# Kernel tuning notes

Measured on AMD Instinct MI355X. Metric: run time of the kernel, lower is better.

Reference implementation:

```python
import jax, jax.numpy as jnp
import numpy as np

DT = 0.1  # module buffer `dt`
I_DIM, H_DIM, BATCH, SEQ = 128, 64, 8, 4096


def setup_inputs() -> dict:
    key = jax.random.key(0)
    ks = jax.random.split(key, 6)
    return {
        "x": jax.random.normal(ks[0], (BATCH, SEQ, I_DIM), dtype=jnp.float32),
        "B": jax.random.uniform(ks[1], (I_DIM, H_DIM), dtype=jnp.float32),
        "C_tilde": jax.random.uniform(ks[2], (I_DIM, H_DIM), dtype=jnp.float32),
        "Lambda": jax.random.uniform(ks[3], (I_DIM, 1, H_DIM), dtype=jnp.float32),
        "P": jax.random.uniform(ks[4], (I_DIM, H_DIM), dtype=jnp.float32),
        "Q": jax.random.uniform(ks[5], (I_DIM, H_DIM), dtype=jnp.float32),
    }


def _compute_K(B, C_tilde, Lambda, P, Q, L):
    # omega_k = exp(2*pi*i*k/L), k = 0..L-1
    n = jnp.arange(L, dtype=jnp.float32)
    omega = jnp.exp((2j * jnp.pi / L) * n).astype(jnp.complex64)          # [L]
    g = (2.0 / DT) * ((1.0 - omega) / (1.0 + omega))                      # [L]
    # denominator: [I, L, H] complex (the big intermediate)
    inv = 1.0 / (g[None, :, None] - Lambda.astype(jnp.complex64))
    a0, a1 = jnp.conj(C_tilde), Q                                          # [I, H]
    b0, b1 = B, P                                                          # [I, H]
    # Cauchy dot products: sum over hidden dim -> [I, L]
    k00 = jnp.einsum('ih,ilh->il', (a0 * b0).astype(jnp.complex64), inv)
    k01 = jnp.einsum('ih,ilh->il', (a0 * b1).astype(jnp.complex64), inv)
    k10 = jnp.einsum('ih,ilh->il', (a1 * b0).astype(jnp.complex64), inv)
    k11 = jnp.einsum('ih,ilh->il', (a1 * b1).astype(jnp.complex64), inv)
    c = 2.0 / (1.0 + omega)                                                # [L]
    K_hat = c[None, :] * (k00 - k01 * (1.0 + k11) * k10)                   # [I, L]
    # irfft crops input along last axis to L//2 + 1 bins (matches torch)
    return jnp.fft.irfft(K_hat, n=L, axis=-1)                              # [I, L] real


def reference(x, B, C_tilde, Lambda, P, Q):
    Bz, L, I = x.shape
    K = _compute_K(B, C_tilde, Lambda, P, Q, L)        # [I, L]
    xt = jnp.transpose(x, (0, 2, 1))                   # [B, I, L]
    n2 = 2 * L
    x_fft = jnp.fft.rfft(xt, n=n2, axis=2)             # zero-pad to 2L -> [B, I, L+1]
    K_fft = jnp.fft.rfft(K, n=n2, axis=1)[None]        # [1, I, L+1]
    y = jnp.fft.irfft(x_fft * K_fft, n=n2, axis=2)[:, :, :L]
    return jnp.transpose(y, (0, 2, 1))                 # [B, L, I]
```

## Files before the change

kernel.cpp:

```cpp
#include <hip/hip_runtime.h>

#define I_DIM 128
#define H_DIM 64
#define BATCH 8
#define SEQ   4096
#define NBIN  (SEQ/2 + 1)
#define NBIN2 (SEQ + 1)

#define SZ(a) ((a) ^ (((a) >> 4) & 15))

__device__ float  g_xT[(size_t)BATCH * I_DIM * SEQ];
__device__ float2 g_Hh[I_DIM * NBIN];
__device__ float2 g_Kf[I_DIM * NBIN2];
__device__ float2 g_Xf[(size_t)BATCH * I_DIM * SEQ];
__device__ float  g_Yt[(size_t)BATCH * I_DIM * SEQ];

__device__ inline float2 cmul(float2 a, float2 b) {
    return make_float2(a.x * b.x - a.y * b.y, a.x * b.y + a.y * b.x);
}
__device__ inline float2 cadd(float2 a, float2 b) { return make_float2(a.x + b.x, a.y + b.y); }
__device__ inline float2 csub(float2 a, float2 b) { return make_float2(a.x - b.x, a.y - b.y); }

__device__ inline void dft8(float2 a[8]) {
    const float C = 0.70710678118654752f;
    float2 s0 = cadd(a[0], a[4]), s1 = cadd(a[1], a[5]);
    float2 s2 = cadd(a[2], a[6]), s3 = cadd(a[3], a[7]);
    float2 d0 = csub(a[0], a[4]), d1 = csub(a[1], a[5]);
    float2 d2 = csub(a[2], a[6]), d3 = csub(a[3], a[7]);
    d1 = make_float2(C * (d1.x + d1.y), C * (d1.y - d1.x));
    d2 = make_float2(d2.y, -d2.x);
    d3 = make_float2(C * (d3.y - d3.x), -C * (d3.x + d3.y));
    {
        float2 p0 = cadd(s0, s2), p1 = cadd(s1, s3);
        float2 m0 = csub(s0, s2), m1 = csub(s1, s3);
        m1 = make_float2(m1.y, -m1.x);
        a[0] = cadd(p0, p1); a[4] = csub(p0, p1);
        a[2] = cadd(m0, m1); a[6] = csub(m0, m1);
    }
    {
        float2 p0 = cadd(d0, d2), p1 = cadd(d1, d3);
        float2 m0 = csub(d0, d2), m1 = csub(d1, d3);
        m1 = make_float2(m1.y, -m1.x);
        a[1] = cadd(p0, p1); a[5] = csub(p0, p1);
        a[3] = cadd(m0, m1); a[7] = csub(m0, m1);
    }
}

__device__ inline void dft4(float2 a[4]) {
    float2 p0 = cadd(a[0], a[2]), p1 = cadd(a[1], a[3]);
    float2 m0 = csub(a[0], a[2]), m1 = csub(a[1], a[3]);
    m1 = make_float2(m1.y, -m1.x);
    a[0] = cadd(p0, p1); a[2] = csub(p0, p1);
    a[1] = cadd(m0, m1); a[3] = csub(m0, m1);
}

template <int N, int S, int NT>
__device__ inline void stage8(float2* __restrict__ lds, int tid) {
    constexpr int NB = N / 8;
    constexpr int ITER = (NB + NT - 1) / NT;
    const bool act = (NB >= NT) || (tid < NB);
    float2 d[ITER][8];
#pragma unroll
    for (int b = 0; b < ITER; ++b) {
        const int u = tid + b * NT;
        if (act) {
#pragma unroll
            for (int j = 0; j < 8; ++j)
                d[b][j] = lds[SZ(u + NB * j)];
        }
    }
    __syncthreads();
#pragma unroll
    for (int b = 0; b < ITER; ++b) {
        const int u = tid + b * NT;
        if (act) {
            const int q = u & (S - 1);
            dft8(d[b]);
            if constexpr (S < NB) {
                const float cang = (float)(-6.283185307179586) / (float)N;
                float sn, cs;
                __sincosf(cang * (float)(u - q), &sn, &cs);
                const float2 w = make_float2(cs, sn);
                float2 t = w;
#pragma unroll
                for (int k = 1; k < 8; ++k) {
                    d[b][k] = cmul(d[b][k], t);
                    if (k < 7) t = cmul(t, w);
                }
            }
            const int base = 8 * u - 7 * q;
#pragma unroll
            for (int k = 0; k < 8; ++k)
                lds[SZ(base + k * S)] = d[b][k];
        }
    }
    __syncthreads();
}

template <int N, int S, int NT>
__device__ inline void stage4(float2* __restrict__ lds, int tid) {
    constexpr int NB = N / 4;
    constexpr int ITER = (NB + NT - 1) / NT;
    const bool act = (NB >= NT) || (tid < NB);
    float2 d[ITER][4];
#pragma unroll
    for (int b = 0; b < ITER; ++b) {
        const int u = tid + b * NT;
        if (act) {
#pragma unroll
            for (int j = 0; j < 4; ++j)
                d[b][j] = lds[SZ(u + NB * j)];
        }
    }
    __syncthreads();
#pragma unroll
    for (int b = 0; b < ITER; ++b) {
        const int u = tid + b * NT;
        if (act) {
            const int q = u & (S - 1);
            dft4(d[b]);
            if constexpr (S < NB) {
                const float cang = (float)(-6.283185307179586) / (float)N;
                float sn, cs;
                __sincosf(cang * (float)(u - q), &sn, &cs);
                const float2 w = make_float2(cs, sn);
                float2 t = w;
#pragma unroll
                for (int k = 1; k < 4; ++k) {
                    d[b][k] = cmul(d[b][k], t);
                    if (k < 3) t = cmul(t, w);
                }
            }
            const int base = 4 * u - 3 * q;
#pragma unroll
            for (int k = 0; k < 4; ++k)
                lds[SZ(base + k * S)] = d[b][k];
        }
    }
    __syncthreads();
}

__device__ inline void halfzero4096_writeback(float2* __restrict__ lds, int tid,
                                              float2 a0, float2 a1,
                                              float2 a2, float2 a3) {
    const float C = 0.70710678118654752f;
    __syncthreads();
    float2 p0 = cadd(a0, a2), p1 = cadd(a1, a3);
    float2 m0 = csub(a0, a2), m1t = csub(a1, a3);
    float2 m1 = make_float2(m1t.y, -m1t.x);
    float2 b0 = cadd(p0, p1), b4 = csub(p0, p1);
    float2 b2 = cadd(m0, m1), b6 = csub(m0, m1);
    float2 c1 = make_float2(C * (a1.x + a1.y), C * (a1.y - a1.x));
    float2 c2 = make_float2(a2.y, -a2.x);
    float2 c3 = make_float2(C * (a3.y - a3.x), -C * (a3.x + a3.y));
    float2 q0 = cadd(a0, c2), q1 = cadd(c1, c3);
    float2 n0 = csub(a0, c2), n1t = csub(c1, c3);
    float2 n1 = make_float2(n1t.y, -n1t.x);
    float2 b1 = cadd(q0, q1), b5 = csub(q0, q1);
    float2 b3 = cadd(n0, n1), b7 = csub(n0, n1);
    float sn, cs;
    __sincosf((float)(-6.283185307179586 / 4096.0) * (float)tid, &sn, &cs);
    float2 w1 = make_float2(cs, sn);
    float2 w2 = cmul(w1, w1), w3 = cmul(w2, w1), w4 = cmul(w2, w2);
    float2 w5 = cmul(w3, w2), w6 = cmul(w3, w3), w7 = cmul(w4, w3);
    const int base = 8 * tid;
    lds[SZ(base + 0)] = b0;
    lds[SZ(base + 1)] = cmul(b1, w1);
    lds[SZ(base + 2)] = cmul(b2, w2);
    lds[SZ(base + 3)] = cmul(b3, w3);
    lds[SZ(base + 4)] = cmul(b4, w4);
    lds[SZ(base + 5)] = cmul(b5, w5);
    lds[SZ(base + 6)] = cmul(b6, w6);
    lds[SZ(base + 7)] = cmul(b7, w7);
    __syncthreads();
}

__device__ inline float2 khat_bin(int i, int k,
                                  const float* __restrict__ Bm,
                                  const float* __restrict__ Cm,
                                  const float* __restrict__ Lm,
                                  const float* __restrict__ Pm,
                                  const float* __restrict__ Qm) {
    float theta = (float)(6.283185307179586 / (double)SEQ) * (float)k;
    float sn, cs;
    sincosf(theta, &sn, &cs);
    float tr = 1.0f - cs, ti = -sn;
    float br = 1.0f + cs, bi = sn;
    float idn = 1.0f / (br * br + bi * bi);
    float gr = 20.0f * (tr * br + ti * bi) * idn;
    float gi = 20.0f * (ti * br - tr * bi) * idn;
    float cr = 2.0f * br * idn;
    float ci = -2.0f * bi * idn;

    const float* Brow = Bm + i * H_DIM;
    const float* Crow = Cm + i * H_DIM;
    const float* Lrow = Lm + i * H_DIM;
    const float* Prow = Pm + i * H_DIM;
    const float* Qrow = Qm + i * H_DIM;

    float k00r = 0.f, k00i = 0.f, k01r = 0.f, k01i = 0.f;
    float k10r = 0.f, k10i = 0.f, k11r = 0.f, k11i = 0.f;
#pragma unroll 8
    for (int h = 0; h < H_DIM; ++h) {
        float lam = Lrow[h];
        float drr = gr - lam;
        float dii = gi;
        float im = 1.0f / (drr * drr + dii * dii);
        float ivr = drr * im;
        float ivi = -dii * im;
        float bv = Brow[h], cv = Crow[h], pv = Prow[h], qv = Qrow[h];
        float cb = cv * bv;
        float cp = cv * pv;
        float qb = qv * bv;
        float qp = qv * pv;
        k00r += cb * ivr; k00i += cb * ivi;
        k01r += cp * ivr; k01i += cp * ivi;
        k10r += qb * ivr; k10i += qb * ivi;
        k11r += qp * ivr; k11i += qp * ivi;
    }
    float t1r = 1.0f + k11r, t1i = k11i;
    float t2r = k01r * t1r - k01i * t1i;
    float t2i = k01r * t1i + k01i * t1r;
    float t3r = t2r * k10r - t2i * k10i;
    float t3i = t2r * k10i + t2i * k10r;
    float nr = k00r - t3r, ni = k00i - t3i;
    return make_float2(cr * nr - ci * ni, cr * ni + ci * nr);
}

__global__ __launch_bounds__(256) void k1_transpose_khat(const float* __restrict__ x,
                                                         const float* __restrict__ Bm,
                                                         const float* __restrict__ Cm,
                                                         const float* __restrict__ Lm,
                                                         const float* __restrict__ Pm,
                                                         const float* __restrict__ Qm) {
    __shared__ float t[64][65];
    const int blk = blockIdx.x;
    const int b = blk >> 7;
    const int rest = blk & 127;
    const int nt = rest >> 1;
    const int it = rest & 1;
    const int tx = threadIdx.x & 63;
    const int ty = threadIdx.x >> 6;
    const int n0 = nt * 64, i0 = it * 64;

    const float* xb = x + (size_t)b * SEQ * I_DIM;
#pragma unroll
    for (int r = 0; r < 16; ++r) {
        int nl = r * 4 + ty;
        t[nl][tx] = xb[(size_t)(n0 + nl) * I_DIM + i0 + tx];
    }
    __syncthreads();
#pragma unroll
    for (int r = 0; r < 16; ++r) {
        int il = r * 4 + ty;
        g_xT[((size_t)b * I_DIM + i0 + il) * SEQ + n0 + tx] = t[tx][il];
    }

    const int ch = blk >> 3, sl = blk & 7;
    const int k = sl * 256 + threadIdx.x;
    g_Hh[(size_t)ch * NBIN + k] = khat_bin(ch, k, Bm, Cm, Lm, Pm, Qm);
    if (sl == 0 && threadIdx.x == 0)
        g_Hh[(size_t)ch * NBIN + 2048] = khat_bin(ch, 2048, Bm, Cm, Lm, Pm, Qm);
}

__global__ __launch_bounds__(512) void k2_kprep_fwd() {
    __shared__ float2 lds[4096];
    const int tid = threadIdx.x;

    if (blockIdx.x < I_DIM) {
        const int i = blockIdx.x;
        const float2* Hrow = g_Hh + (size_t)i * NBIN;
#pragma unroll
        for (int r = 0; r < 4; ++r) {
            int m = tid + (r << 9);
            float2 Hm = Hrow[m];
            float2 Hc = Hrow[2048 - m];
            float pr = Hm.x + Hc.x, pi2 = Hm.y - Hc.y;
            float dr = Hm.x - Hc.x, di = Hm.y + Hc.y;
            float sn, cs;
            __sincosf((float)(3.141592653589793 / 2048.0) * (float)m, &sn, &cs);
            float Or = 0.5f * (cs * dr - sn * di);
            float Oi = 0.5f * (sn * dr + cs * di);
            lds[SZ(m)] = make_float2(0.5f * pr - Oi, -(0.5f * pi2 + Or));
        }
        __syncthreads();

        stage4<2048, 1,   512>(lds, tid);
        stage8<2048, 4,   512>(lds, tid);
        stage8<2048, 32,  512>(lds, tid);
        stage8<2048, 256, 512>(lds, tid);

        const float s1 = 1.0f / 2048.0f;
        float2 a[4];
#pragma unroll
        for (int j = 0; j < 4; ++j) {
            float2 o = lds[SZ(tid + (j << 9))];
            a[j] = make_float2(o.x * s1, -o.y * s1);
        }
        halfzero4096_writeback(lds, tid, a[0], a[1], a[2], a[3]);

        stage8<4096, 8,   512>(lds, tid);
        stage8<4096, 64,  512>(lds, tid);
        stage8<4096, 512, 512>(lds, tid);

        float2* Kfrow = g_Kf + (size_t)i * NBIN2;
#pragma unroll
        for (int r = 0; r < 9; ++r) {
            int m = tid + (r << 9);
            if (m <= 4096) {
                float2 Zq = lds[SZ(m & 4095)];
                float2 Zr = lds[SZ((4096 - m) & 4095)];
                float sn, cs;
                __sincosf((float)(-3.141592653589793 / 4096.0) * (float)m, &sn, &cs);
                float pr = Zq.x + Zr.x, pi2 = Zq.y - Zr.y;
                float dr = Zq.x - Zr.x, di = Zq.y + Zr.y;
                float jt_r = -sn * dr - cs * di;
                float jt_i =  cs * dr - sn * di;
                Kfrow[m] = make_float2(0.5f * (pr - jt_r), 0.5f * (pi2 - jt_i));
            }
        }
    } else {
        const int blk = blockIdx.x - I_DIM;
        const int b = blk & 7;
        const int i = blk >> 3;

        const float2* xrow = (const float2*)(g_xT + ((size_t)b * I_DIM + i) * SEQ);
        float2 a0 = xrow[tid];
        float2 a1 = xrow[tid + 512];
        float2 a2 = xrow[tid + 1024];
        float2 a3 = xrow[tid + 1536];
        halfzero4096_writeback(lds, tid, a0, a1, a2, a3);

        stage8<4096, 8,  512>(lds, tid);
        stage8<4096, 64, 512>(lds, tid);

        float2 e[8];
#pragma unroll
        for (int j = 0; j < 8; ++j) e[j] = lds[SZ(tid + (j << 9))];
        dft8(e);
        float2* dst = g_Xf + (size_t)blk * SEQ;
#pragma unroll
        for (int k = 0; k < 8; ++k)
            dst[tid + (k << 9)] = e[k];
    }
}

__global__ __launch_bounds__(512) void k3_combine_inv() {
    __shared__ float2 lds[4096];
    const int tid = threadIdx.x;
    const int blk = blockIdx.x;
    const int b = blk & 7;
    const int i = blk >> 3;
    const float2* Xf = g_Xf + (size_t)blk * SEQ;
    const float2* Kfrow = g_Kf + (size_t)i * NBIN2;

    float2 d[8];
#pragma unroll
    for (int j = 0; j < 8; ++j) {
        int m = tid + (j << 9);
        int mm = (4096 - m) & 4095;
        float2 Zq = Xf[m];
        float2 Zr = Xf[mm];
        float2 Km  = Kfrow[m];
        float2 Km2 = Kfrow[4096 - m];
        float sn, cs;
        __sincosf((float)(-3.141592653589793 / 4096.0) * (float)m, &sn, &cs);
        float pr = Zq.x + Zr.x, pi2 = Zq.y - Zr.y;
        float dr = Zq.x - Zr.x, di = Zq.y + Zr.y;
        float jt_r = -sn * dr - cs * di;
        float jt_i =  cs * dr - sn * di;
        float2 Xm  = make_float2(0.5f * (pr - jt_r),  0.5f * ( pi2 - jt_i));
        float2 Xm2 = make_float2(0.5f * (pr + jt_r),  0.5f * (-pi2 - jt_i));
        float2 Ym  = cmul(Xm,  Km);
        float2 Ym2 = cmul(Xm2, Km2);
        float qr = Ym.x + Ym2.x, qi = Ym.y - Ym2.y;
        float er = Ym.x - Ym2.x, ei = Ym.y + Ym2.y;
        float gr2 = sn * er - cs * ei;
        float gi2 = sn * ei + cs * er;
        d[j] = make_float2(0.5f * (qr + gr2), -0.5f * (qi + gi2));
    }

    dft8(d);
    {
        float sn, cs;
        __sincosf((float)(-6.283185307179586 / 4096.0) * (float)tid, &sn, &cs);
        float2 w1 = make_float2(cs, sn);
        float2 w2 = cmul(w1, w1), w3 = cmul(w2, w1), w4 = cmul(w2, w2);
        float2 w5 = cmul(w3, w2), w6 = cmul(w3, w3), w7 = cmul(w4, w3);
        d[1] = cmul(d[1], w1); d[2] = cmul(d[2], w2); d[3] = cmul(d[3], w3);
        d[4] = cmul(d[4], w4); d[5] = cmul(d[5], w5); d[6] = cmul(d[6], w6);
        d[7] = cmul(d[7], w7);
    }
    const int base = 8 * tid;
#pragma unroll
    for (int k = 0; k < 8; ++k) lds[SZ(base + k)] = d[k];
    __syncthreads();

    stage8<4096, 8,  512>(lds, tid);
    stage8<4096, 64, 512>(lds, tid);

    float2 e[8];
#pragma unroll
    for (int j = 0; j < 8; ++j) e[j] = lds[SZ(tid + (j << 9))];
    dft8(e);
    const float inv = 1.0f / 4096.0f;
    float2* yrow = (float2*)(g_Yt + ((size_t)b * I_DIM + i) * SEQ);
#pragma unroll
    for (int k = 0; k < 4; ++k)
        yrow[tid + (k << 9)] = make_float2(e[k].x * inv, -e[k].y * inv);
}

__global__ __launch_bounds__(256) void k4_transpose_out(float* __restrict__ y) {
    __shared__ float t[64][65];
    const int blk = blockIdx.x;
    const int b = blk >> 7;
    const int rest = blk & 127;
    const int nt = rest >> 1;
    const int it = rest & 1;
    const int tx = threadIdx.x & 63;
    const int ty = threadIdx.x >> 6;
    const int n0 = nt * 64, i0 = it * 64;

#pragma unroll
    for (int r = 0; r < 16; ++r) {
        int il = r * 4 + ty;
        t[il][tx] = g_Yt[((size_t)b * I_DIM + i0 + il) * SEQ + n0 + tx];
    }
    __syncthreads();
    float* yb = y + (size_t)b * SEQ * I_DIM;
#pragma unroll
    for (int r = 0; r < 16; ++r) {
        int nl = r * 4 + ty;
        yb[(size_t)(n0 + nl) * I_DIM + i0 + tx] = t[tx][nl];
    }
}

extern "C" void kernel_launch(void* const* d_in, const int* in_sizes, int n_in,
                              void* d_out, int out_size, void* d_ws, size_t ws_size,
                              hipStream_t stream) {
    const float* x  = (const float*)d_in[0];
    const float* Bm = (const float*)d_in[1];
    const float* Cm = (const float*)d_in[2];
    const float* Lm = (const float*)d_in[3];
    const float* Pm = (const float*)d_in[4];
    const float* Qm = (const float*)d_in[5];
    float* out = (float*)d_out;

    k1_transpose_khat<<<1024, 256, 0, stream>>>(x, Bm, Cm, Lm, Pm, Qm);
    k2_kprep_fwd<<<I_DIM + BATCH * I_DIM, 512, 0, stream>>>();
    k3_combine_inv<<<BATCH * I_DIM, 512, 0, stream>>>();
    k4_transpose_out<<<1024, 256, 0, stream>>>(out);
}
```

Measured before the change: 72.17 us.

## Pack two real channels per complex FFT instead of real-FFT half-length trick

Replaces the half-length real-FFT packing (one real row as a 4096-point complex FFT plus post-twiddle) with a two-for-one scheme: channel g and g+64 are packed as real and imaginary parts of one 8192-point complex FFT, and their spectra are split by conjugate symmetry. The kernel-spectrum, forward-x and inverse passes all switch to 8192-point transforms with 64KB of LDS, and the block count halves. This drops the separate twiddle pre- and post-processing passes and gives each block more work, at the cost of doubled LDS per block (lower occupancy), an extra radix stage, and more scattered conjugate-index global reads.

```diff
diff --git a/kernel.cpp b/kernel.cpp
--- a/kernel.cpp
+++ b/kernel.cpp
@@ -46,14 +46,6 @@
     }
 }
 
-__device__ inline void dft4(float2 a[4]) {
-    float2 p0 = cadd(a[0], a[2]), p1 = cadd(a[1], a[3]);
-    float2 m0 = csub(a[0], a[2]), m1 = csub(a[1], a[3]);
-    m1 = make_float2(m1.y, -m1.x);
-    a[0] = cadd(p0, p1); a[2] = csub(p0, p1);
-    a[1] = cadd(m0, m1); a[3] = csub(m0, m1);
-}
-
 template <int N, int S, int NT>
 __device__ inline void stage8(float2* __restrict__ lds, int tid) {
     constexpr int NB = N / 8;
@@ -97,54 +89,11 @@
     __syncthreads();
 }
 
-template <int N, int S, int NT>
-__device__ inline void stage4(float2* __restrict__ lds, int tid) {
-    constexpr int NB = N / 4;
-    constexpr int ITER = (NB + NT - 1) / NT;
-    const bool act = (NB >= NT) || (tid < NB);
-    float2 d[ITER][4];
-#pragma unroll
-    for (int b = 0; b < ITER; ++b) {
-        const int u = tid + b * NT;
-        if (act) {
-#pragma unroll
-            for (int j = 0; j < 4; ++j)
-                d[b][j] = lds[SZ(u + NB * j)];
-        }
-    }
-    __syncthreads();
-#pragma unroll
-    for (int b = 0; b < ITER; ++b) {
-        const int u = tid + b * NT;
-        if (act) {
-            const int q = u & (S - 1);
-            dft4(d[b]);
-            if constexpr (S < NB) {
-                const float cang = (float)(-6.283185307179586) / (float)N;
-                float sn, cs;
-                __sincosf(cang * (float)(u - q), &sn, &cs);
-                const float2 w = make_float2(cs, sn);
-                float2 t = w;
-#pragma unroll
-                for (int k = 1; k < 4; ++k) {
-                    d[b][k] = cmul(d[b][k], t);
-                    if (k < 3) t = cmul(t, w);
-                }
-            }
-            const int base = 4 * u - 3 * q;
-#pragma unroll
-            for (int k = 0; k < 4; ++k)
-                lds[SZ(base + k * S)] = d[b][k];
-        }
-    }
-    __syncthreads();
-}
-
-__device__ inline void halfzero4096_writeback(float2* __restrict__ lds, int tid,
-                                              float2 a0, float2 a1,
-                                              float2 a2, float2 a3) {
+template <int N>
+__device__ inline void halfzero_s1_write(float2* __restrict__ lds, int u,
+                                         float2 a0, float2 a1,
+                                         float2 a2, float2 a3) {
     const float C = 0.70710678118654752f;
-    __syncthreads();
     float2 p0 = cadd(a0, a2), p1 = cadd(a1, a3);
     float2 m0 = csub(a0, a2), m1t = csub(a1, a3);
     float2 m1 = make_float2(m1t.y, -m1t.x);
@@ -159,11 +108,11 @@
     float2 b1 = cadd(q0, q1), b5 = csub(q0, q1);
     float2 b3 = cadd(n0, n1), b7 = csub(n0, n1);
     float sn, cs;
-    __sincosf((float)(-6.283185307179586 / 4096.0) * (float)tid, &sn, &cs);
+    __sincosf((float)(-6.283185307179586) / (float)N * (float)u, &sn, &cs);
     float2 w1 = make_float2(cs, sn);
     float2 w2 = cmul(w1, w1), w3 = cmul(w2, w1), w4 = cmul(w2, w2);
     float2 w5 = cmul(w3, w2), w6 = cmul(w3, w3), w7 = cmul(w4, w3);
-    const int base = 8 * tid;
+    const int base = 8 * u;
     lds[SZ(base + 0)] = b0;
     lds[SZ(base + 1)] = cmul(b1, w1);
     lds[SZ(base + 2)] = cmul(b2, w2);
@@ -172,7 +121,25 @@
     lds[SZ(base + 5)] = cmul(b5, w5);
     lds[SZ(base + 6)] = cmul(b6, w6);
     lds[SZ(base + 7)] = cmul(b7, w7);
-    __syncthreads();
+}
+
+template <int N>
+__device__ inline void full_s1_write(float2* __restrict__ lds, int u, float2 d[8]) {
+    dft8(d);
+    float sn, cs;
+    __sincosf((float)(-6.283185307179586) / (float)N * (float)u, &sn, &cs);
+    float2 w1 = make_float2(cs, sn);
+    float2 w2 = cmul(w1, w1), w3 = cmul(w2, w1), w4 = cmul(w2, w2);
+    float2 w5 = cmul(w3, w2), w6 = cmul(w3, w3), w7 = cmul(w4, w3);
+    const int base = 8 * u;
+    lds[SZ(base + 0)] = d[0];
+    lds[SZ(base + 1)] = cmul(d[1], w1);
+    lds[SZ(base + 2)] = cmul(d[2], w2);
+    lds[SZ(base + 3)] = cmul(d[3], w3);
+    lds[SZ(base + 4)] = cmul(d[4], w4);
+    lds[SZ(base + 5)] = cmul(d[5], w5);
+    lds[SZ(base + 6)] = cmul(d[6], w6);
+    lds[SZ(base + 7)] = cmul(d[7], w7);
 }
 
 __device__ inline float2 khat_bin(int i, int k,
@@ -264,150 +231,166 @@
 }
 
 __global__ __launch_bounds__(512) void k2_kprep_fwd() {
-    __shared__ float2 lds[4096];
+    __shared__ float2 L[8192];
     const int tid = threadIdx.x;
 
-    if (blockIdx.x < I_DIM) {
-        const int i = blockIdx.x;
-        const float2* Hrow = g_Hh + (size_t)i * NBIN;
-#pragma unroll
-        for (int r = 0; r < 4; ++r) {
+    if (blockIdx.x < 64) {
+        const int g = blockIdx.x;
+        const float2* HA = g_Hh + (size_t)g * NBIN;
+        const float2* HB = g_Hh + (size_t)(g + 64) * NBIN;
+
+        float2 d[8];
+#pragma unroll
+        for (int j = 0; j < 8; ++j) {
+            int m = tid + (j << 9);
+            float2 hA, hB;
+            if (m <= 2048) { hA = HA[m]; hB = HB[m]; }
+            else {
+                float2 tA = HA[4096 - m], tB = HB[4096 - m];
+                hA = make_float2(tA.x, -tA.y);
+                hB = make_float2(tB.x, -tB.y);
+            }
+            d[j] = make_float2(hA.x - hB.y, -(hA.y + hB.x));
+        }
+        full_s1_write<4096>(L, tid, d);
+        __syncthreads();
+
+        stage8<4096, 8,   512>(L, tid);
+        stage8<4096, 64,  512>(L, tid);
+        stage8<4096, 512, 512>(L, tid);
+
+        const float s1 = 1.0f / 4096.0f;
+        float2 va[2][4];
+#pragma unroll
+        for (int b2 = 0; b2 < 2; ++b2)
+#pragma unroll
+            for (int j = 0; j < 4; ++j) {
+                int n = tid + (b2 << 9) + (j << 10);
+                float2 o = L[SZ(n)];
+                va[b2][j] = make_float2(o.x * s1, -o.y * s1);
+            }
+        __syncthreads();
+#pragma unroll
+        for (int b2 = 0; b2 < 2; ++b2)
+            halfzero_s1_write<8192>(L, tid + (b2 << 9),
+                                    va[b2][0], va[b2][1], va[b2][2], va[b2][3]);
+        __syncthreads();
+
+        stage8<8192, 8,   512>(L, tid);
+        stage8<8192, 64,  512>(L, tid);
+        stage8<8192, 512, 512>(L, tid);
+
+        float2* KfA = g_Kf + (size_t)g * NBIN2;
+        float2* KfB = g_Kf + (size_t)(g + 64) * NBIN2;
+#pragma unroll
+        for (int r = 0; r < 8; ++r) {
             int m = tid + (r << 9);
-            float2 Hm = Hrow[m];
-            float2 Hc = Hrow[2048 - m];
-            float pr = Hm.x + Hc.x, pi2 = Hm.y - Hc.y;
-            float dr = Hm.x - Hc.x, di = Hm.y + Hc.y;
-            float sn, cs;
-            __sincosf((float)(3.141592653589793 / 2048.0) * (float)m, &sn, &cs);
-            float Or = 0.5f * (cs * dr - sn * di);
-            float Oi = 0.5f * (sn * dr + cs * di);
-            lds[SZ(m)] = make_float2(0.5f * pr - Oi, -(0.5f * pi2 + Or));
-        }
+            float2 A0 = L[SZ(m)], A1 = L[SZ(m + 4096)];
+            float2 P = cadd(A0, A1);
+            float2 Q;
+            if (m == 0) Q = P;
+            else {
+                float2 B0 = L[SZ(4096 - m)], B1 = L[SZ(8192 - m)];
+                Q = csub(B0, B1);
+            }
+            KfA[m] = make_float2(0.5f * (P.x + Q.x), 0.5f * (P.y - Q.y));
+            float dxr = P.x - Q.x, dyr = P.y + Q.y;
+            KfB[m] = make_float2(0.5f * dyr, -0.5f * dxr);
+        }
+        if (tid == 0) {
+            float2 P = csub(L[SZ(0)], L[SZ(4096)]);
+            KfA[4096] = make_float2(P.x, 0.f);
+            KfB[4096] = make_float2(P.y, 0.f);
+        }
+    } else {
+        const int blk = blockIdx.x - 64;
+        const int b = blk & 7;
+        const int g = blk >> 3;
+        const float* xrA = g_xT + ((size_t)b * I_DIM + g) * SEQ;
+        const float* xrB = g_xT + ((size_t)b * I_DIM + g + 64) * SEQ;
+
+        float2 va[2][4];
+#pragma unroll
+        for (int b2 = 0; b2 < 2; ++b2)
+#pragma unroll
+            for (int j = 0; j < 4; ++j) {
+                int n = tid + (b2 << 9) + (j << 10);
+                va[b2][j] = make_float2(xrA[n], xrB[n]);
+            }
+#pragma unroll
+        for (int b2 = 0; b2 < 2; ++b2)
+            halfzero_s1_write<8192>(L, tid + (b2 << 9),
+                                    va[b2][0], va[b2][1], va[b2][2], va[b2][3]);
         __syncthreads();
 
-        stage4<2048, 1,   512>(lds, tid);
-        stage8<2048, 4,   512>(lds, tid);
-        stage8<2048, 32,  512>(lds, tid);
-        stage8<2048, 256, 512>(lds, tid);
-
-        const float s1 = 1.0f / 2048.0f;
-        float2 a[4];
-#pragma unroll
-        for (int j = 0; j < 4; ++j) {
-            float2 o = lds[SZ(tid + (j << 9))];
-            a[j] = make_float2(o.x * s1, -o.y * s1);
-        }
-        halfzero4096_writeback(lds, tid, a[0], a[1], a[2], a[3]);
-
-        stage8<4096, 8,   512>(lds, tid);
-        stage8<4096, 64,  512>(lds, tid);
-        stage8<4096, 512, 512>(lds, tid);
-
-        float2* Kfrow = g_Kf + (size_t)i * NBIN2;
-#pragma unroll
-        for (int r = 0; r < 9; ++r) {
-            int m = tid + (r << 9);
-            if (m <= 4096) {
-                float2 Zq = lds[SZ(m & 4095)];
-                float2 Zr = lds[SZ((4096 - m) & 4095)];
-                float sn, cs;
-                __sincosf((float)(-3.141592653589793 / 4096.0) * (float)m, &sn, &cs);
-                float pr = Zq.x + Zr.x, pi2 = Zq.y - Zr.y;
-                float dr = Zq.x - Zr.x, di = Zq.y + Zr.y;
-                float jt_r = -sn * dr - cs * di;
-                float jt_i =  cs * dr - sn * di;
-                Kfrow[m] = make_float2(0.5f * (pr - jt_r), 0.5f * (pi2 - jt_i));
-            }
-        }
-    } else {
-        const int blk = blockIdx.x - I_DIM;
-        const int b = blk & 7;
-        const int i = blk >> 3;
-
-        const float2* xrow = (const float2*)(g_xT + ((size_t)b * I_DIM + i) * SEQ);
-        float2 a0 = xrow[tid];
-        float2 a1 = xrow[tid + 512];
-        float2 a2 = xrow[tid + 1024];
-        float2 a3 = xrow[tid + 1536];
-        halfzero4096_writeback(lds, tid, a0, a1, a2, a3);
-
-        stage8<4096, 8,  512>(lds, tid);
-        stage8<4096, 64, 512>(lds, tid);
-
-        float2 e[8];
-#pragma unroll
-        for (int j = 0; j < 8; ++j) e[j] = lds[SZ(tid + (j << 9))];
-        dft8(e);
-        float2* dst = g_Xf + (size_t)blk * SEQ;
-#pragma unroll
-        for (int k = 0; k < 8; ++k)
-            dst[tid + (k << 9)] = e[k];
+        stage8<8192, 8,   512>(L, tid);
+        stage8<8192, 64,  512>(L, tid);
+        stage8<8192, 512, 512>(L, tid);
+
+        float2* dst = g_Xf + (size_t)blk * 2 * SEQ;
+#pragma unroll
+        for (int r = 0; r < 8; ++r) {
+            int u = tid + (r << 9);
+            float2 A0 = L[SZ(u)], A1 = L[SZ(u + 4096)];
+            dst[u]        = cadd(A0, A1);
+            dst[u + 4096] = csub(A0, A1);
+        }
     }
 }
 
 __global__ __launch_bounds__(512) void k3_combine_inv() {
-    __shared__ float2 lds[4096];
+    __shared__ float2 L[8192];
     const int tid = threadIdx.x;
     const int blk = blockIdx.x;
     const int b = blk & 7;
-    const int i = blk >> 3;
-    const float2* Xf = g_Xf + (size_t)blk * SEQ;
-    const float2* Kfrow = g_Kf + (size_t)i * NBIN2;
-
-    float2 d[8];
-#pragma unroll
-    for (int j = 0; j < 8; ++j) {
-        int m = tid + (j << 9);
-        int mm = (4096 - m) & 4095;
-        float2 Zq = Xf[m];
-        float2 Zr = Xf[mm];
-        float2 Km  = Kfrow[m];
-        float2 Km2 = Kfrow[4096 - m];
-        float sn, cs;
-        __sincosf((float)(-3.141592653589793 / 4096.0) * (float)m, &sn, &cs);
-        float pr = Zq.x + Zr.x, pi2 = Zq.y - Zr.y;
-        float dr = Zq.x - Zr.x, di = Zq.y + Zr.y;
-        float jt_r = -sn * dr - cs * di;
-        float jt_i =  cs * dr - sn * di;
-        float2 Xm  = make_float2(0.5f * (pr - jt_r),  0.5f * ( pi2 - jt_i));
-        float2 Xm2 = make_float2(0.5f * (pr + jt_r),  0.5f * (-pi2 - jt_i));
-        float2 Ym  = cmul(Xm,  Km);
-        float2 Ym2 = cmul(Xm2, Km2);
-        float qr = Ym.x + Ym2.x, qi = Ym.y - Ym2.y;
-        float er = Ym.x - Ym2.x, ei = Ym.y + Ym2.y;
-        float gr2 = sn * er - cs * ei;
-        float gi2 = sn * ei + cs * er;
-        d[j] = make_float2(0.5f * (qr + gr2), -0.5f * (qi + gi2));
-    }
-
-    dft8(d);
-    {
-        float sn, cs;
-        __sincosf((float)(-6.283185307179586 / 4096.0) * (float)tid, &sn, &cs);
-        float2 w1 = make_float2(cs, sn);
-        float2 w2 = cmul(w1, w1), w3 = cmul(w2, w1), w4 = cmul(w2, w2);
-        float2 w5 = cmul(w3, w2), w6 = cmul(w3, w3), w7 = cmul(w4, w3);
-        d[1] = cmul(d[1], w1); d[2] = cmul(d[2], w2); d[3] = cmul(d[3], w3);
-        d[4] = cmul(d[4], w4); d[5] = cmul(d[5], w5); d[6] = cmul(d[6], w6);
-        d[7] = cmul(d[7], w7);
-    }
-    const int base = 8 * tid;
-#pragma unroll
-    for (int k = 0; k < 8; ++k) lds[SZ(base + k)] = d[k];
+    const int g = blk >> 3;
+    const float2* Z = g_Xf + (size_t)blk * 2 * SEQ;
+    const float2* KfA = g_Kf + (size_t)g * NBIN2;
+    const float2* KfB = g_Kf + (size_t)(g + 64) * NBIN2;
+
+    float2 d[2][8];
+#pragma unroll
+    for (int b2 = 0; b2 < 2; ++b2) {
+        const int u = tid + (b2 << 9);
+#pragma unroll
+        for (int j = 0; j < 8; ++j) {
+            int m = u + (j << 10);
+            float2 P = Z[m];
+            float2 Q = (m == 0) ? P : Z[8192 - m];
+            float2 XA = make_float2(0.5f * (P.x + Q.x), 0.5f * (P.y - Q.y));
+            float dxr = P.x - Q.x, dyr = P.y + Q.y;
+            float2 XB = make_float2(0.5f * dyr, -0.5f * dxr);
+            float2 KA, KB;
+            if (m <= 4096) { KA = KfA[m]; KB = KfB[m]; }
+            else {
+                float2 tA = KfA[8192 - m], tB = KfB[8192 - m];
+                KA = make_float2(tA.x, -tA.y);
+                KB = make_float2(tB.x, -tB.y);
+            }
+            float2 YA = cmul(XA, KA);
+            float2 YB = cmul(XB, KB);
+            d[b2][j] = make_float2(YA.x - YB.y, -(YA.y + YB.x));
+        }
+    }
+#pragma unroll
+    for (int b2 = 0; b2 < 2; ++b2)
+        full_s1_write<8192>(L, tid + (b2 << 9), d[b2]);
     __syncthreads();
 
-    stage8<4096, 8,  512>(lds, tid);
-    stage8<4096, 64, 512>(lds, tid);
-
-    float2 e[8];
-#pragma unroll
-    for (int j = 0; j < 8; ++j) e[j] = lds[SZ(tid + (j << 9))];
-    dft8(e);
-    const float inv = 1.0f / 4096.0f;
-    float2* yrow = (float2*)(g_Yt + ((size_t)b * I_DIM + i) * SEQ);
-#pragma unroll
-    for (int k = 0; k < 4; ++k)
-        yrow[tid + (k << 9)] = make_float2(e[k].x * inv, -e[k].y * inv);
+    stage8<8192, 8,   512>(L, tid);
+    stage8<8192, 64,  512>(L, tid);
+    stage8<8192, 512, 512>(L, tid);
+
+    const float inv = 1.0f / 8192.0f;
+    float* yA = g_Yt + ((size_t)b * I_DIM + g) * SEQ;
+    float* yB = g_Yt + ((size_t)b * I_DIM + g + 64) * SEQ;
+#pragma unroll
+    for (int r = 0; r < 8; ++r) {
+        int n = tid + (r << 9);
+        float2 F = cadd(L[SZ(n)], L[SZ(n + 4096)]);
+        yA[n] = F.x * inv;
+        yB[n] = -F.y * inv;
+    }
 }
 
 __global__ __launch_bounds__(256) void k4_transpose_out(float* __restrict__ y) {
@@ -447,7 +430,7 @@
     float* out = (float*)d_out;
 
     k1_transpose_khat<<<1024, 256, 0, stream>>>(x, Bm, Cm, Lm, Pm, Qm);
-    k2_kprep_fwd<<<I_DIM + BATCH * I_DIM, 512, 0, stream>>>();
-    k3_combine_inv<<<BATCH * I_DIM, 512, 0, stream>>>();
+    k2_kprep_fwd<<<64 + 512, 512, 0, stream>>>();
+    k3_combine_inv<<<512, 512, 0, stream>>>();
     k4_transpose_out<<<1024, 256, 0, stream>>>(out);
 }
```

Result: slower. 82.91 us (+14.9%).

## Switch 4096-point FFTs to radix-16 stages with 256-thread blocks

Applied to the files above, without the earlier changes.

Replaces the radix-8/radix-4 LDS FFT stages with radix-16 stages run by 256 threads, cutting the number of LDS round trips and barriers per 4096-point transform from about three to two. The K spectrum path is restructured: a 4096-point inverse of the Hermitian half-spectrum, followed by a twiddled forward transform that only fills the odd bins, while even bins are copied straight from Hh. The LDS swizzle gains an extra XOR term to avoid bank conflicts at the larger strides. Each thread now holds 16 complex values, which raises register pressure and may reduce occupancy.

```diff
diff --git a/kernel.cpp b/kernel.cpp
--- a/kernel.cpp
+++ b/kernel.cpp
@@ -7,7 +7,7 @@
 #define NBIN  (SEQ/2 + 1)
 #define NBIN2 (SEQ + 1)
 
-#define SZ(a) ((a) ^ (((a) >> 4) & 15))
+#define SZ(a) ((a) ^ (((a) >> 4) & 15) ^ (((a) >> 8) & 15))
 
 __device__ float  g_xT[(size_t)BATCH * I_DIM * SEQ];
 __device__ float2 g_Hh[I_DIM * NBIN];
@@ -46,132 +46,105 @@
     }
 }
 
-__device__ inline void dft4(float2 a[4]) {
-    float2 p0 = cadd(a[0], a[2]), p1 = cadd(a[1], a[3]);
-    float2 m0 = csub(a[0], a[2]), m1 = csub(a[1], a[3]);
-    m1 = make_float2(m1.y, -m1.x);
-    a[0] = cadd(p0, p1); a[2] = csub(p0, p1);
-    a[1] = cadd(m0, m1); a[3] = csub(m0, m1);
-}
-
-template <int N, int S, int NT>
-__device__ inline void stage8(float2* __restrict__ lds, int tid) {
-    constexpr int NB = N / 8;
-    constexpr int ITER = (NB + NT - 1) / NT;
-    const bool act = (NB >= NT) || (tid < NB);
-    float2 d[ITER][8];
-#pragma unroll
-    for (int b = 0; b < ITER; ++b) {
-        const int u = tid + b * NT;
-        if (act) {
-#pragma unroll
-            for (int j = 0; j < 8; ++j)
-                d[b][j] = lds[SZ(u + NB * j)];
-        }
-    }
-    __syncthreads();
-#pragma unroll
-    for (int b = 0; b < ITER; ++b) {
-        const int u = tid + b * NT;
-        if (act) {
-            const int q = u & (S - 1);
-            dft8(d[b]);
-            if constexpr (S < NB) {
-                const float cang = (float)(-6.283185307179586) / (float)N;
-                float sn, cs;
-                __sincosf(cang * (float)(u - q), &sn, &cs);
-                const float2 w = make_float2(cs, sn);
-                float2 t = w;
-#pragma unroll
-                for (int k = 1; k < 8; ++k) {
-                    d[b][k] = cmul(d[b][k], t);
-                    if (k < 7) t = cmul(t, w);
-                }
-            }
-            const int base = 8 * u - 7 * q;
-#pragma unroll
-            for (int k = 0; k < 8; ++k)
-                lds[SZ(base + k * S)] = d[b][k];
-        }
-    }
-    __syncthreads();
-}
-
-template <int N, int S, int NT>
-__device__ inline void stage4(float2* __restrict__ lds, int tid) {
-    constexpr int NB = N / 4;
-    constexpr int ITER = (NB + NT - 1) / NT;
-    const bool act = (NB >= NT) || (tid < NB);
-    float2 d[ITER][4];
-#pragma unroll
-    for (int b = 0; b < ITER; ++b) {
-        const int u = tid + b * NT;
-        if (act) {
-#pragma unroll
-            for (int j = 0; j < 4; ++j)
-                d[b][j] = lds[SZ(u + NB * j)];
-        }
-    }
-    __syncthreads();
-#pragma unroll
-    for (int b = 0; b < ITER; ++b) {
-        const int u = tid + b * NT;
-        if (act) {
-            const int q = u & (S - 1);
-            dft4(d[b]);
-            if constexpr (S < NB) {
-                const float cang = (float)(-6.283185307179586) / (float)N;
-                float sn, cs;
-                __sincosf(cang * (float)(u - q), &sn, &cs);
-                const float2 w = make_float2(cs, sn);
-                float2 t = w;
-#pragma unroll
-                for (int k = 1; k < 4; ++k) {
-                    d[b][k] = cmul(d[b][k], t);
-                    if (k < 3) t = cmul(t, w);
-                }
-            }
-            const int base = 4 * u - 3 * q;
-#pragma unroll
-            for (int k = 0; k < 4; ++k)
-                lds[SZ(base + k * S)] = d[b][k];
-        }
-    }
-    __syncthreads();
-}
-
-__device__ inline void halfzero4096_writeback(float2* __restrict__ lds, int tid,
-                                              float2 a0, float2 a1,
-                                              float2 a2, float2 a3) {
+__device__ inline void dft8hz(float2 x0, float2 x1, float2 x2, float2 x3,
+                              float2 b[8]) {
     const float C = 0.70710678118654752f;
-    __syncthreads();
-    float2 p0 = cadd(a0, a2), p1 = cadd(a1, a3);
-    float2 m0 = csub(a0, a2), m1t = csub(a1, a3);
+    float2 p0 = cadd(x0, x2), p1 = cadd(x1, x3);
+    float2 m0 = csub(x0, x2), m1t = csub(x1, x3);
     float2 m1 = make_float2(m1t.y, -m1t.x);
-    float2 b0 = cadd(p0, p1), b4 = csub(p0, p1);
-    float2 b2 = cadd(m0, m1), b6 = csub(m0, m1);
-    float2 c1 = make_float2(C * (a1.x + a1.y), C * (a1.y - a1.x));
-    float2 c2 = make_float2(a2.y, -a2.x);
-    float2 c3 = make_float2(C * (a3.y - a3.x), -C * (a3.x + a3.y));
-    float2 q0 = cadd(a0, c2), q1 = cadd(c1, c3);
-    float2 n0 = csub(a0, c2), n1t = csub(c1, c3);
+    b[0] = cadd(p0, p1); b[4] = csub(p0, p1);
+    b[2] = cadd(m0, m1); b[6] = csub(m0, m1);
+    float2 c1 = make_float2(C * (x1.x + x1.y), C * (x1.y - x1.x));
+    float2 c2 = make_float2(x2.y, -x2.x);
+    float2 c3 = make_float2(C * (x3.y - x3.x), -C * (x3.x + x3.y));
+    float2 q0 = cadd(x0, c2), q1 = cadd(c1, c3);
+    float2 n0 = csub(x0, c2), n1t = csub(c1, c3);
     float2 n1 = make_float2(n1t.y, -n1t.x);
-    float2 b1 = cadd(q0, q1), b5 = csub(q0, q1);
-    float2 b3 = cadd(n0, n1), b7 = csub(n0, n1);
+    b[1] = cadd(q0, q1); b[5] = csub(q0, q1);
+    b[3] = cadd(n0, n1); b[7] = csub(n0, n1);
+}
+
+__device__ inline void combine16(const float2 e[8], const float2 o[8],
+                                 float2 b[16]) {
+    const float C  = 0.70710678118654752f;
+    const float C1 = 0.92387953251128674f;
+    const float S1 = 0.38268343236508977f;
+    float2 t;
+    b[0] = cadd(e[0], o[0]);  b[8]  = csub(e[0], o[0]);
+    t = cmul(o[1], make_float2( C1, -S1)); b[1] = cadd(e[1], t); b[9]  = csub(e[1], t);
+    t = cmul(o[2], make_float2(  C,  -C)); b[2] = cadd(e[2], t); b[10] = csub(e[2], t);
+    t = cmul(o[3], make_float2( S1, -C1)); b[3] = cadd(e[3], t); b[11] = csub(e[3], t);
+    t = make_float2(o[4].y, -o[4].x);      b[4] = cadd(e[4], t); b[12] = csub(e[4], t);
+    t = cmul(o[5], make_float2(-S1, -C1)); b[5] = cadd(e[5], t); b[13] = csub(e[5], t);
+    t = cmul(o[6], make_float2( -C,  -C)); b[6] = cadd(e[6], t); b[14] = csub(e[6], t);
+    t = cmul(o[7], make_float2(-C1, -S1)); b[7] = cadd(e[7], t); b[15] = csub(e[7], t);
+}
+
+__device__ inline void dft16(float2 a[16]) {
+    float2 e[8] = {a[0], a[2], a[4], a[6], a[8], a[10], a[12], a[14]};
+    float2 o[8] = {a[1], a[3], a[5], a[7], a[9], a[11], a[13], a[15]};
+    dft8(e); dft8(o);
+    combine16(e, o, a);
+}
+
+__device__ inline void s1_twiddle_write(float2* __restrict__ lds, int u,
+                                        float2 b[16]) {
     float sn, cs;
-    __sincosf((float)(-6.283185307179586 / 4096.0) * (float)tid, &sn, &cs);
+    __sincosf((float)(-6.283185307179586 / 4096.0) * (float)u, &sn, &cs);
     float2 w1 = make_float2(cs, sn);
     float2 w2 = cmul(w1, w1), w3 = cmul(w2, w1), w4 = cmul(w2, w2);
     float2 w5 = cmul(w3, w2), w6 = cmul(w3, w3), w7 = cmul(w4, w3);
-    const int base = 8 * tid;
-    lds[SZ(base + 0)] = b0;
-    lds[SZ(base + 1)] = cmul(b1, w1);
-    lds[SZ(base + 2)] = cmul(b2, w2);
-    lds[SZ(base + 3)] = cmul(b3, w3);
-    lds[SZ(base + 4)] = cmul(b4, w4);
-    lds[SZ(base + 5)] = cmul(b5, w5);
-    lds[SZ(base + 6)] = cmul(b6, w6);
-    lds[SZ(base + 7)] = cmul(b7, w7);
+    float2 w8 = cmul(w4, w4);
+    const int base = 16 * u;
+    lds[SZ(base + 0)]  = b[0];
+    lds[SZ(base + 1)]  = cmul(b[1], w1);
+    lds[SZ(base + 2)]  = cmul(b[2], w2);
+    lds[SZ(base + 3)]  = cmul(b[3], w3);
+    lds[SZ(base + 4)]  = cmul(b[4], w4);
+    lds[SZ(base + 5)]  = cmul(b[5], w5);
+    lds[SZ(base + 6)]  = cmul(b[6], w6);
+    lds[SZ(base + 7)]  = cmul(b[7], w7);
+    lds[SZ(base + 8)]  = cmul(b[8], w8);
+    lds[SZ(base + 9)]  = cmul(cmul(b[9],  w1), w8);
+    lds[SZ(base + 10)] = cmul(cmul(b[10], w2), w8);
+    lds[SZ(base + 11)] = cmul(cmul(b[11], w3), w8);
+    lds[SZ(base + 12)] = cmul(cmul(b[12], w4), w8);
+    lds[SZ(base + 13)] = cmul(cmul(b[13], w5), w8);
+    lds[SZ(base + 14)] = cmul(cmul(b[14], w6), w8);
+    lds[SZ(base + 15)] = cmul(cmul(b[15], w7), w8);
+}
+
+template <int S>
+__device__ inline void stage16(float2* __restrict__ lds, int u) {
+    float2 d[16];
+#pragma unroll
+    for (int j = 0; j < 16; ++j) d[j] = lds[SZ(u + 256 * j)];
+    __syncthreads();
+    const int q = u & (S - 1);
+    dft16(d);
+    if constexpr (S < 256) {
+        float sn, cs;
+        __sincosf((float)(-6.283185307179586 / 4096.0) * (float)(u - q), &sn, &cs);
+        float2 w1 = make_float2(cs, sn);
+        float2 w2 = cmul(w1, w1), w3 = cmul(w2, w1), w4 = cmul(w2, w2);
+        float2 w5 = cmul(w3, w2), w6 = cmul(w3, w3), w7 = cmul(w4, w3);
+        float2 w8 = cmul(w4, w4);
+        d[1]  = cmul(d[1], w1);  d[2]  = cmul(d[2], w2);
+        d[3]  = cmul(d[3], w3);  d[4]  = cmul(d[4], w4);
+        d[5]  = cmul(d[5], w5);  d[6]  = cmul(d[6], w6);
+        d[7]  = cmul(d[7], w7);  d[8]  = cmul(d[8], w8);
+        d[9]  = cmul(cmul(d[9],  w1), w8);
+        d[10] = cmul(cmul(d[10], w2), w8);
+        d[11] = cmul(cmul(d[11], w3), w8);
+        d[12] = cmul(cmul(d[12], w4), w8);
+        d[13] = cmul(cmul(d[13], w5), w8);
+        d[14] = cmul(cmul(d[14], w6), w8);
+        d[15] = cmul(cmul(d[15], w7), w8);
+    }
+    const int base = 16 * u - 15 * q;
+#pragma unroll
+    for (int k = 0; k < 16; ++k)
+        lds[SZ(base + k * S)] = d[k];
     __syncthreads();
 }
 
@@ -263,101 +236,110 @@
         g_Hh[(size_t)ch * NBIN + 2048] = khat_bin(ch, 2048, Bm, Cm, Lm, Pm, Qm);
 }
 
-__global__ __launch_bounds__(512) void k2_kprep_fwd() {
-    __shared__ float2 lds[4096];
-    const int tid = threadIdx.x;
+__global__ __launch_bounds__(256) void k2_kprep_fwd() {
+    __shared__ float2 L[4096];
+    const int u = threadIdx.x;
 
     if (blockIdx.x < I_DIM) {
         const int i = blockIdx.x;
         const float2* Hrow = g_Hh + (size_t)i * NBIN;
-#pragma unroll
-        for (int r = 0; r < 4; ++r) {
-            int m = tid + (r << 9);
-            float2 Hm = Hrow[m];
-            float2 Hc = Hrow[2048 - m];
-            float pr = Hm.x + Hc.x, pi2 = Hm.y - Hc.y;
-            float dr = Hm.x - Hc.x, di = Hm.y + Hc.y;
-            float sn, cs;
-            __sincosf((float)(3.141592653589793 / 2048.0) * (float)m, &sn, &cs);
-            float Or = 0.5f * (cs * dr - sn * di);
-            float Oi = 0.5f * (sn * dr + cs * di);
-            lds[SZ(m)] = make_float2(0.5f * pr - Oi, -(0.5f * pi2 + Or));
+
+        {
+            float2 d[16];
+#pragma unroll
+            for (int j = 0; j < 16; ++j) {
+                int m = u + (j << 8);
+                float2 h;
+                if (m <= 2048) h = Hrow[m];
+                else { float2 tt = Hrow[4096 - m]; h = make_float2(tt.x, -tt.y); }
+                d[j] = make_float2(h.x, -h.y);
+            }
+            dft16(d);
+            s1_twiddle_write(L, u, d);
+            __syncthreads();
         }
-        __syncthreads();
-
-        stage4<2048, 1,   512>(lds, tid);
-        stage8<2048, 4,   512>(lds, tid);
-        stage8<2048, 32,  512>(lds, tid);
-        stage8<2048, 256, 512>(lds, tid);
-
-        const float s1 = 1.0f / 2048.0f;
-        float2 a[4];
-#pragma unroll
-        for (int j = 0; j < 4; ++j) {
-            float2 o = lds[SZ(tid + (j << 9))];
-            a[j] = make_float2(o.x * s1, -o.y * s1);
+        stage16<16>(L, u);
+        stage16<256>(L, u);
+
+        {
+            const float2 W32[16] = {
+                make_float2( 1.00000000f,  0.00000000f), make_float2( 0.98078528f, -0.19509032f),
+                make_float2( 0.92387953f, -0.38268343f), make_float2( 0.83146961f, -0.55557023f),
+                make_float2( 0.70710678f, -0.70710678f), make_float2( 0.55557023f, -0.83146961f),
+                make_float2( 0.38268343f, -0.92387953f), make_float2( 0.19509032f, -0.98078528f),
+                make_float2( 0.00000000f, -1.00000000f), make_float2(-0.19509032f, -0.98078528f),
+                make_float2(-0.38268343f, -0.92387953f), make_float2(-0.55557023f, -0.83146961f),
+                make_float2(-0.70710678f, -0.70710678f), make_float2(-0.83146961f, -0.55557023f),
+                make_float2(-0.92387953f, -0.38268343f), make_float2(-0.98078528f, -0.19509032f)};
+            float snu, csu;
+            __sincosf((float)(-3.141592653589793 / 4096.0) * (float)u, &snu, &csu);
+            float2 wu = make_float2(csu, snu);
+            float2 v[16];
+#pragma unroll
+            for (int j = 0; j < 16; ++j) {
+                float kr = L[SZ(u + (j << 8))].x * (1.0f / 4096.0f);
+                float2 w = cmul(wu, W32[j]);
+                v[j] = make_float2(kr * w.x, kr * w.y);
+            }
+            __syncthreads();
+            dft16(v);
+            s1_twiddle_write(L, u, v);
+            __syncthreads();
         }
-        halfzero4096_writeback(lds, tid, a[0], a[1], a[2], a[3]);
-
-        stage8<4096, 8,   512>(lds, tid);
-        stage8<4096, 64,  512>(lds, tid);
-        stage8<4096, 512, 512>(lds, tid);
-
+        stage16<16>(L, u);
+
+        float2 e[16];
+#pragma unroll
+        for (int j = 0; j < 16; ++j) e[j] = L[SZ(u + (j << 8))];
+        dft16(e);
         float2* Kfrow = g_Kf + (size_t)i * NBIN2;
 #pragma unroll
-        for (int r = 0; r < 9; ++r) {
-            int m = tid + (r << 9);
-            if (m <= 4096) {
-                float2 Zq = lds[SZ(m & 4095)];
-                float2 Zr = lds[SZ((4096 - m) & 4095)];
-                float sn, cs;
-                __sincosf((float)(-3.141592653589793 / 4096.0) * (float)m, &sn, &cs);
-                float pr = Zq.x + Zr.x, pi2 = Zq.y - Zr.y;
-                float dr = Zq.x - Zr.x, di = Zq.y + Zr.y;
-                float jt_r = -sn * dr - cs * di;
-                float jt_i =  cs * dr - sn * di;
-                Kfrow[m] = make_float2(0.5f * (pr - jt_r), 0.5f * (pi2 - jt_i));
-            }
-        }
+        for (int k = 0; k < 8; ++k)
+            Kfrow[2 * (u + (k << 8)) + 1] = e[k];
+        for (int r = u; r <= 2048; r += 256)
+            Kfrow[2 * r] = Hrow[r];
     } else {
         const int blk = blockIdx.x - I_DIM;
         const int b = blk & 7;
         const int i = blk >> 3;
-
         const float2* xrow = (const float2*)(g_xT + ((size_t)b * I_DIM + i) * SEQ);
-        float2 a0 = xrow[tid];
-        float2 a1 = xrow[tid + 512];
-        float2 a2 = xrow[tid + 1024];
-        float2 a3 = xrow[tid + 1536];
-        halfzero4096_writeback(lds, tid, a0, a1, a2, a3);
-
-        stage8<4096, 8,  512>(lds, tid);
-        stage8<4096, 64, 512>(lds, tid);
-
-        float2 e[8];
-#pragma unroll
-        for (int j = 0; j < 8; ++j) e[j] = lds[SZ(tid + (j << 9))];
-        dft8(e);
+
+        float2 xx[8];
+#pragma unroll
+        for (int j = 0; j < 8; ++j) xx[j] = xrow[u + (j << 8)];
+        float2 e[8], o[8], bb[16];
+        dft8hz(xx[0], xx[2], xx[4], xx[6], e);
+        dft8hz(xx[1], xx[3], xx[5], xx[7], o);
+        combine16(e, o, bb);
+        s1_twiddle_write(L, u, bb);
+        __syncthreads();
+
+        stage16<16>(L, u);
+
+        float2 f[16];
+#pragma unroll
+        for (int j = 0; j < 16; ++j) f[j] = L[SZ(u + (j << 8))];
+        dft16(f);
         float2* dst = g_Xf + (size_t)blk * SEQ;
 #pragma unroll
-        for (int k = 0; k < 8; ++k)
-            dst[tid + (k << 9)] = e[k];
-    }
-}
-
-__global__ __launch_bounds__(512) void k3_combine_inv() {
-    __shared__ float2 lds[4096];
-    const int tid = threadIdx.x;
+        for (int k = 0; k < 16; ++k)
+            dst[u + (k << 8)] = f[k];
+    }
+}
+
+__global__ __launch_bounds__(256) void k3_combine_inv() {
+    __shared__ float2 L[4096];
+    const int u = threadIdx.x;
     const int blk = blockIdx.x;
     const int b = blk & 7;
     const int i = blk >> 3;
     const float2* Xf = g_Xf + (size_t)blk * SEQ;
     const float2* Kfrow = g_Kf + (size_t)i * NBIN2;
 
-    float2 d[8];
-#pragma unroll
-    for (int j = 0; j < 8; ++j) {
-        int m = tid + (j << 9);
+    float2 d[16];
+#pragma unroll
+    for (int j = 0; j < 16; ++j) {
+        int m = u + (j << 8);
         int mm = (4096 - m) & 4095;
         float2 Zq = Xf[m];
         float2 Zr = Xf[mm];
@@ -379,35 +361,21 @@
         float gi2 = sn * ei + cs * er;
         d[j] = make_float2(0.5f * (qr + gr2), -0.5f * (qi + gi2));
     }
-
-    dft8(d);
-    {
-        float sn, cs;
-        __sincosf((float)(-6.283185307179586 / 4096.0) * (float)tid, &sn, &cs);
-        float2 w1 = make_float2(cs, sn);
-        float2 w2 = cmul(w1, w1), w3 = cmul(w2, w1), w4 = cmul(w2, w2);
-        float2 w5 = cmul(w3, w2), w6 = cmul(w3, w3), w7 = cmul(w4, w3);
-        d[1] = cmul(d[1], w1); d[2] = cmul(d[2], w2); d[3] = cmul(d[3], w3);
-        d[4] = cmul(d[4], w4); d[5] = cmul(d[5], w5); d[6] = cmul(d[6], w6);
-        d[7] = cmul(d[7], w7);
-    }
-    const int base = 8 * tid;
-#pragma unroll
-    for (int k = 0; k < 8; ++k) lds[SZ(base + k)] = d[k];
+    dft16(d);
+    s1_twiddle_write(L, u, d);
     __syncthreads();
 
-    stage8<4096, 8,  512>(lds, tid);
-    stage8<4096, 64, 512>(lds, tid);
-
-    float2 e[8];
-#pragma unroll
-    for (int j = 0; j < 8; ++j) e[j] = lds[SZ(tid + (j << 9))];
-    dft8(e);
+    stage16<16>(L, u);
+
+    float2 e[16];
+#pragma unroll
+    for (int j = 0; j < 16; ++j) e[j] = L[SZ(u + (j << 8))];
+    dft16(e);
     const float inv = 1.0f / 4096.0f;
     float2* yrow = (float2*)(g_Yt + ((size_t)b * I_DIM + i) * SEQ);
 #pragma unroll
-    for (int k = 0; k < 4; ++k)
-        yrow[tid + (k << 9)] = make_float2(e[k].x * inv, -e[k].y * inv);
+    for (int k = 0; k < 8; ++k)
+        yrow[u + (k << 8)] = make_float2(e[k].x * inv, -e[k].y * inv);
 }
 
 __global__ __launch_bounds__(256) void k4_transpose_out(float* __restrict__ y) {
@@ -447,7 +415,7 @@
     float* out = (float*)d_out;
 
     k1_transpose_khat<<<1024, 256, 0, stream>>>(x, Bm, Cm, Lm, Pm, Qm);
-    k2_kprep_fwd<<<I_DIM + BATCH * I_DIM, 512, 0, stream>>>();
-    k3_combine_inv<<<BATCH * I_DIM, 512, 0, stream>>>();
+    k2_kprep_fwd<<<I_DIM + BATCH * I_DIM, 256, 0, stream>>>();
+    k3_combine_inv<<<BATCH * I_DIM, 256, 0, stream>>>();
     k4_transpose_out<<<1024, 256, 0, stream>>>(out);
 }
```

New measurement: 71.68 us. Within noise of the previous version (-0.7%).
